# Optimization experiments

Measured on AMD Instinct MI355X. Metric: run time of the kernel, lower is better.

Reference implementation:

```python
import jax, jax.numpy as jnp
import numpy as np

B, S, D = 8, 4096, 512
EPS = 1e-6


def setup_inputs() -> dict:
    key = jax.random.key(0)
    ks = jax.random.split(key, 9)
    scale = 1.0 / np.sqrt(D)
    inp = {
        "x_seq": jax.random.normal(ks[0], (B, S, D), dtype=jnp.float32),
        "Wq": jax.random.uniform(ks[1], (D, D), jnp.float32, -scale, scale),
        "bq": jax.random.uniform(ks[2], (D,), jnp.float32, -scale, scale),
        "Wk": jax.random.uniform(ks[3], (D, D), jnp.float32, -scale, scale),
        "bk": jax.random.uniform(ks[4], (D,), jnp.float32, -scale, scale),
        "Wv": jax.random.uniform(ks[5], (D, D), jnp.float32, -scale, scale),
        "bv": jax.random.uniform(ks[6], (D,), jnp.float32, -scale, scale),
        "Wa": jax.random.uniform(ks[7], (D, D), jnp.float32, -scale, scale),
        "ba": jax.random.uniform(ks[8], (D,), jnp.float32, -scale, scale),
    }
    return inp


def _forward(x_seq, Wq, bq, Wk, bk, Wv, bv, Wa, ba):
    # Precompute all projections for the whole sequence (big GEMMs).
    q = jax.nn.relu(jnp.einsum('bsd,ed->bse', x_seq, Wq) + bq)  # phi = relu
    k = jax.nn.relu(jnp.einsum('bsd,ed->bse', x_seq, Wk) + bk)
    v = jnp.einsum('bsd,ed->bse', x_seq, Wv) + bv
    a = jax.nn.sigmoid(jnp.einsum('bsd,ed->bse', x_seq, Wa) + ba)

    # time-major for scan: (S, B, D)
    qs, ks_, vs, as_ = (jnp.swapaxes(t, 0, 1) for t in (q, k, v, a))

    def step(carry, inp):
        s, z = carry                      # s: (B,D,D), z: (B,D)
        q_t, k_t, v_t, a_t = inp
        s = a_t[:, :, None] * s + k_t[:, :, None] * v_t[:, None, :]
        z = a_t * z + k_t
        num = jnp.einsum('bi,bij->bj', q_t, s)
        den = jnp.sum(q_t * z, axis=-1, keepdims=True) + EPS
        return (s, z), num / den

    s0 = jnp.zeros((x_seq.shape[0], x_seq.shape[2], x_seq.shape[2]), x_seq.dtype)
    z0 = jnp.zeros((x_seq.shape[0], x_seq.shape[2]), x_seq.dtype)
    _, ys = jax.lax.scan(step, (s0, z0), (qs, ks_, vs, as_))
    return jnp.swapaxes(ys, 0, 1)  # (B, S, D)


def reference(x_seq, Wq, bq, Wk, bk, Wv, bv, Wa, ba):
    return _forward(x_seq, Wq, bq, Wk, bk, Wv, bv, Wa, ba)
```

## Files before the change

### kernel.cpp

```cpp
#include <hip/hip_runtime.h>
#include <hip/hip_bf16.h>
#include <cstdint>
#include <cstddef>

#define D_DIM 512
#define B_DIM 8
#define S_DIM 4096
#define M_DIM (B_DIM * S_DIM)
#define CHUNK 64
#define NCHUNK (S_DIM / CHUNK)
#define NSEG 8
#define CSEG (NCHUNK / NSEG)
#define EPS_C 1e-6f

typedef __attribute__((ext_vector_type(8))) short bf16x8;
typedef __attribute__((ext_vector_type(4))) float f32x4;

#define GLOAD_LDS16(src, dst)                                              \
  __builtin_amdgcn_global_load_lds(                                        \
      (const __attribute__((address_space(1))) void*)(src),                \
      (__attribute__((address_space(3))) void*)(dst), 16, 0, 0)

__device__ __forceinline__ unsigned short f2bf(float f) {
  uint32_t u = __float_as_uint(f);
  u = (u + 0x7fffu + ((u >> 16) & 1u)) >> 16;
  return (unsigned short)u;
}
__device__ __forceinline__ float bf2f(unsigned short s) { return __uint_as_float(((uint32_t)s) << 16); }

__global__ void cvt_f32_bf16(const float* __restrict__ in, unsigned short* __restrict__ out, int n4) {
  int i = blockIdx.x * blockDim.x + threadIdx.x;
  int stride = gridDim.x * blockDim.x;
  for (; i < n4; i += stride) {
    float4 f = ((const float4*)in)[i];
    ushort4 o;
    o.x = f2bf(f.x); o.y = f2bf(f.y); o.z = f2bf(f.z); o.w = f2bf(f.w);
    ((ushort4*)out)[i] = o;
  }
}

#define PTM 256
#define PTN 256
#define PBK 64

__global__ __launch_bounds__(512, 2) void proj_gemm(
    const unsigned short* __restrict__ Xb,
    const unsigned short* __restrict__ Wb,
    const float* __restrict__ bq, const float* __restrict__ bk,
    const float* __restrict__ bv, const float* __restrict__ ba,
    unsigned short* __restrict__ q_ws, unsigned short* __restrict__ k_ws,
    unsigned short* __restrict__ v_ws, unsigned short* __restrict__ g_ws) {
  __shared__ unsigned short SB[2 * (PTM + PTN) * PBK];

  const int proj = blockIdx.z;
  const unsigned short* W = Wb + (size_t)proj * D_DIM * D_DIM;
  const int m0 = blockIdx.x * PTM;
  const int n0 = blockIdx.y * PTN;
  const int lane = threadIdx.x & 63;
  const int w = threadIdx.x >> 6;
  const int l16 = lane & 15, q4 = lane >> 4;
  const int wm = (w >> 2) * 128;
  const int wn = (w & 3) * 64;

  f32x4 acc[8][4];
#pragma unroll
  for (int m = 0; m < 8; ++m)
#pragma unroll
    for (int n = 0; n < 4; ++n) acc[m][n] = (f32x4){0.f, 0.f, 0.f, 0.f};

  const int srow = lane >> 3;
  const int sg = lane & 7;

  auto STAGE = [&](int buf, int kc) {
    unsigned short* A = SB + buf * ((PTM + PTN) * PBK);
    unsigned short* Bs = A + PTM * PBK;
#pragma unroll
    for (int q = 0; q < 4; ++q) {
      const int row = w * 32 + q * 8 + srow;
      const int g = sg ^ (row & 7);
      GLOAD_LDS16(&Xb[(size_t)(m0 + row) * D_DIM + kc + g * 8], &A[(w * 32 + q * 8) * PBK]);
      GLOAD_LDS16(&W[(size_t)(n0 + row) * D_DIM + kc + g * 8], &Bs[(w * 32 + q * 8) * PBK]);
    }
  };

  STAGE(0, 0);
  __syncthreads();

  for (int t = 0; t < D_DIM / PBK; ++t) {
    const int cur = t & 1;
    if (t + 1 < D_DIM / PBK) STAGE(cur ^ 1, (t + 1) * PBK);

    const unsigned short* A = SB + cur * ((PTM + PTN) * PBK);
    const unsigned short* Bs = A + PTM * PBK;
    const int rsw = l16 & 7;
#pragma unroll
    for (int ks = 0; ks < 2; ++ks) {
      const int gphys = ((ks * 4 + q4) ^ rsw) * 8;
      bf16x8 afr[8], bfr[4];
#pragma unroll
      for (int m = 0; m < 8; ++m)
        afr[m] = *(const bf16x8*)&A[(wm + m * 16 + l16) * PBK + gphys];
#pragma unroll
      for (int n = 0; n < 4; ++n)
        bfr[n] = *(const bf16x8*)&Bs[(wn + n * 16 + l16) * PBK + gphys];
#pragma unroll
      for (int m = 0; m < 8; ++m)
#pragma unroll
        for (int n = 0; n < 4; ++n)
          acc[m][n] = __builtin_amdgcn_mfma_f32_16x16x32_bf16(afr[m], bfr[n], acc[m][n], 0, 0, 0);
    }
    __syncthreads();
  }

  const float* bias = (proj == 0) ? bq : (proj == 1) ? bk : (proj == 2) ? bv : ba;
  unsigned short* outp = (proj == 0) ? q_ws : (proj == 1) ? k_ws : (proj == 2) ? v_ws : g_ws;
  const bool do_relu = (proj <= 1);
  unsigned short* EP = &SB[w * 128 * 32];

#pragma unroll
  for (int p = 0; p < 2; ++p) {
#pragma unroll
    for (int half = 0; half < 2; ++half) {
      const int in_idx = p * 2 + half;
      const int nn = n0 + wn + in_idx * 16 + l16;
      const float bn = bias[nn];
#pragma unroll
      for (int m = 0; m < 8; ++m) {
#pragma unroll
        for (int vv = 0; vv < 4; ++vv) {
          float val = acc[m][in_idx][vv] + bn;
          if (do_relu) val = fmaxf(val, 0.f);
          EP[(m * 16 + q4 * 4 + vv) * 32 + half * 16 + l16] = f2bf(val);
        }
      }
    }
#pragma unroll
    for (int it = 0; it < 8; ++it) {
      const int row = it * 16 + (lane >> 2);
      const int ccol = (lane & 3) * 8;
      bf16x8 vdat = *(const bf16x8*)&EP[row * 32 + ccol];
      size_t gidx = (size_t)(m0 + wm + row) * D_DIM + (size_t)(n0 + wn + p * 32 + ccol);
      *(bf16x8*)&outp[gidx] = vdat;
    }
  }
}

__global__ __launch_bounds__(512) void prep(
    const unsigned short* __restrict__ q, const unsigned short* __restrict__ k,
    const unsigned short* __restrict__ g,
    unsigned short* __restrict__ qt, unsigned short* __restrict__ kt,
    unsigned short* __restrict__ kh,
    float* __restrict__ Af, float* __restrict__ khs) {
  __shared__ float segp[8][512];
  const int c = blockIdx.x, b = blockIdx.y;
  const int seg = threadIdx.x >> 6;
  const int t = threadIdx.x & 63;
  const int i0 = t * 8;
  const int r0 = seg * 8;
  const size_t t0 = (size_t)b * S_DIM + (size_t)c * CHUNK;
  const size_t cb = ((size_t)b * NCHUNK + c) * D_DIM;

  float sp[8];
#pragma unroll
  for (int j = 0; j < 8; ++j) sp[j] = 1.f;
  for (int r = 0; r < 8; ++r) {
    bf16x8 gv = *(const bf16x8*)&g[(t0 + r0 + r) * D_DIM + i0];
#pragma unroll
    for (int j = 0; j < 8; ++j)
      sp[j] *= 1.f / (1.f + __expf(-bf2f((unsigned short)gv[j])));
  }
  *(float4*)&segp[seg][i0] = *(float4*)&sp[0];
  *(float4*)&segp[seg][i0 + 4] = *(float4*)&sp[4];
  __syncthreads();

  float pre[8], tot[8];
#pragma unroll
  for (int j = 0; j < 8; ++j) { pre[j] = 1.f; tot[j] = 1.f; }
  for (int s2 = 0; s2 < 8; ++s2) {
    float4 v0 = *(const float4*)&segp[s2][i0];
    float4 v1 = *(const float4*)&segp[s2][i0 + 4];
    float v[8] = {v0.x, v0.y, v0.z, v0.w, v1.x, v1.y, v1.z, v1.w};
#pragma unroll
    for (int j = 0; j < 8; ++j) {
      tot[j] *= v[j];
      if (s2 < seg) pre[j] *= v[j];
    }
  }
  if (seg == 0) {
    float4 a0 = {tot[0], tot[1], tot[2], tot[3]};
    float4 a1 = {tot[4], tot[5], tot[6], tot[7]};
    *(float4*)&Af[cb + i0] = a0;
    *(float4*)&Af[cb + i0 + 4] = a1;
  }

  float cum[8], ssum[8];
#pragma unroll
  for (int j = 0; j < 8; ++j) { cum[j] = pre[j]; ssum[j] = 0.f; }
  for (int r = 0; r < 8; ++r) {
    size_t idx = (t0 + r0 + r) * D_DIM + i0;
    bf16x8 gv = *(const bf16x8*)&g[idx];
    bf16x8 qv8 = *(const bf16x8*)&q[idx];
    bf16x8 kv8 = *(const bf16x8*)&k[idx];
    bf16x8 oq, ok, okh;
#pragma unroll
    for (int j = 0; j < 8; ++j) {
      cum[j] *= 1.f / (1.f + __expf(-bf2f((unsigned short)gv[j])));
      float qv = bf2f((unsigned short)qv8[j]);
      float kv = bf2f((unsigned short)kv8[j]);
      oq[j] = (short)f2bf(qv * cum[j]);
      float inv = 1.f / cum[j];
      ok[j] = (short)f2bf(kv * inv);
      float khf = kv * (tot[j] * inv);
      okh[j] = (short)f2bf(khf);
      ssum[j] += khf;
    }
    *(bf16x8*)&qt[idx] = oq;
    *(bf16x8*)&kt[idx] = ok;
    *(bf16x8*)&kh[idx] = okh;
  }

  __syncthreads();
  *(float4*)&segp[seg][i0] = *(float4*)&ssum[0];
  *(float4*)&segp[seg][i0 + 4] = *(float4*)&ssum[4];
  __syncthreads();
  if (seg == 0) {
    float s[8];
#pragma unroll
    for (int j = 0; j < 8; ++j) s[j] = 0.f;
    for (int s2 = 0; s2 < 8; ++s2) {
      float4 v0 = *(const float4*)&segp[s2][i0];
      float4 v1 = *(const float4*)&segp[s2][i0 + 4];
      s[0] += v0.x; s[1] += v0.y; s[2] += v0.z; s[3] += v0.w;
      s[4] += v1.x; s[5] += v1.y; s[6] += v1.z; s[7] += v1.w;
    }
    float4 a0 = {s[0], s[1], s[2], s[3]};
    float4 a1 = {s[4], s[5], s[6], s[7]};
    *(float4*)&khs[cb + i0] = a0;
    *(float4*)&khs[cb + i0 + 4] = a1;
  }
}

__global__ __launch_bounds__(256) void transpose_cd(
    const unsigned short* __restrict__ in, unsigned short* __restrict__ outT) {
  __shared__ unsigned short tile[CHUNK][264];
  const int c = blockIdx.x, b = blockIdx.y;
  const size_t base_in = ((size_t)b * S_DIM + (size_t)c * CHUNK) * D_DIM;
  const size_t base_out = ((size_t)b * NCHUNK + c) * (size_t)D_DIM * CHUNK;
  const int tid = threadIdx.x;
#pragma unroll
  for (int h = 0; h < 2; ++h) {
    if (h) __syncthreads();
#pragma unroll
    for (int it = 0; it < 8; ++it) {
      int flat = (it * 256 + tid) * 8;
      int row = flat >> 8;
      int col = flat & 255;
      *(uint4*)&tile[row][col] = *(const uint4*)&in[base_in + (size_t)row * D_DIM + h * 256 + col];
    }
    __syncthreads();
#pragma unroll
    for (int it = 0; it < 8; ++it) {
      int wq = it * 256 + tid;
      int i_loc = wq >> 3;
      int r0 = (wq & 7) * 8;
      ushort4 v0, v1;
      v0.x = tile[r0 + 0][i_loc]; v0.y = tile[r0 + 1][i_loc];
      v0.z = tile[r0 + 2][i_loc]; v0.w = tile[r0 + 3][i_loc];
      v1.x = tile[r0 + 4][i_loc]; v1.y = tile[r0 + 5][i_loc];
      v1.z = tile[r0 + 6][i_loc]; v1.w = tile[r0 + 7][i_loc];
      size_t o = base_out + (size_t)(h * 256 + i_loc) * CHUNK + r0;
      *(ushort4*)&outT[o] = v0;
      *(ushort4*)&outT[o + 4] = v1;
    }
  }
}

__global__ __launch_bounds__(256) void intra(
    const unsigned short* __restrict__ qt, const unsigned short* kt,
    const unsigned short* __restrict__ VT,
    unsigned short* numI, float* __restrict__ rs) {
  __shared__ unsigned short P_lds[CHUNK][CHUNK + 8];
  const int c = blockIdx.x, b = blockIdx.y;
  const size_t t0 = (size_t)b * S_DIM + (size_t)c * CHUNK;
  const int lane = threadIdx.x & 63, w = threadIdx.x >> 6;
  const int l16 = lane & 15, q4 = lane >> 4;

  f32x4 accP[4];
#pragma unroll
  for (int n = 0; n < 4; ++n) accP[n] = (f32x4){0.f, 0.f, 0.f, 0.f};
#pragma unroll
  for (int ks = 0; ks < 16; ++ks) {
    bf16x8 afr = *(const bf16x8*)&qt[(t0 + 16 * w + l16) * D_DIM + 32 * ks + 8 * q4];
#pragma unroll
    for (int n = 0; n < 4; ++n) {
      bf16x8 bfr = *(const bf16x8*)&kt[(t0 + 16 * n + l16) * D_DIM + 32 * ks + 8 * q4];
      accP[n] = __builtin_amdgcn_mfma_f32_16x16x32_bf16(afr, bfr, accP[n], 0, 0, 0);
    }
  }
  float rsum[4] = {0.f, 0.f, 0.f, 0.f};
#pragma unroll
  for (int n = 0; n < 4; ++n) {
    int m = 16 * n + l16;
#pragma unroll
    for (int vv = 0; vv < 4; ++vv) {
      int r = 16 * w + 4 * q4 + vv;
      float pv = (m <= r) ? accP[n][vv] : 0.f;
      rsum[vv] += pv;
      P_lds[r][m] = f2bf(pv);
    }
  }
#pragma unroll
  for (int msk = 1; msk < 16; msk <<= 1) {
#pragma unroll
    for (int vv = 0; vv < 4; ++vv) rsum[vv] += __shfl_xor(rsum[vv], msk, 64);
  }
  if (l16 == 0) {
#pragma unroll
    for (int vv = 0; vv < 4; ++vv) rs[t0 + 16 * w + 4 * q4 + vv] = rsum[vv];
  }
  __syncthreads();
  bf16x8 pa0 = *(const bf16x8*)&P_lds[16 * w + l16][8 * q4];
  bf16x8 pa1 = *(const bf16x8*)&P_lds[16 * w + l16][32 + 8 * q4];
  const size_t vtb = ((size_t)b * NCHUNK + c) * (size_t)D_DIM * CHUNK;
#pragma unroll 4
  for (int nt = 0; nt < 32; ++nt) {
    bf16x8 b0 = *(const bf16x8*)&VT[vtb + (size_t)(nt * 16 + l16) * CHUNK + 8 * q4];
    bf16x8 b1 = *(const bf16x8*)&VT[vtb + (size_t)(nt * 16 + l16) * CHUNK + 32 + 8 * q4];
    f32x4 acc = (f32x4){0.f, 0.f, 0.f, 0.f};
    acc = __builtin_amdgcn_mfma_f32_16x16x32_bf16(pa0, b0, acc, 0, 0, 0);
    acc = __builtin_amdgcn_mfma_f32_16x16x32_bf16(pa1, b1, acc, 0, 0, 0);
#pragma unroll
    for (int vv = 0; vv < 4; ++vv)
      numI[(t0 + 16 * w + 4 * q4 + vv) * D_DIM + nt * 16 + l16] = f2bf(acc[vv]);
  }
}

__global__ __launch_bounds__(512) void zscan(
    const float* __restrict__ Af, const float* __restrict__ khs,
    float* __restrict__ zall, float* __restrict__ Pseg) {
  const int b = blockIdx.x;
  const int i = threadIdx.x;
  float z = 0.f, rp = 1.f;
  for (int c = 0; c < NCHUNK; ++c) {
    const size_t cb = ((size_t)b * NCHUNK + c) * D_DIM;
    zall[cb + i] = z;
    float af = Af[cb + i];
    z = fmaf(af, z, khs[cb + i]);
    rp *= af;
    if ((c & (CSEG - 1)) == CSEG - 1) {
      Pseg[((size_t)b * NSEG + (c / CSEG)) * D_DIM + i] = rp;
      rp = 1.f;
    }
  }
}

__global__ __launch_bounds__(512) void denk(
    const unsigned short* __restrict__ qt, const float* __restrict__ zall,
    float* rs_invden) {
  const int c = blockIdx.x, b = blockIdx.y;
  const int lane = threadIdx.x & 63, w = threadIdx.x >> 6;
  const size_t t0 = (size_t)b * S_DIM + (size_t)c * CHUNK;
  const size_t zb = ((size_t)b * NCHUNK + c) * D_DIM;
  float4 z0 = *(const float4*)&zall[zb + lane * 8];
  float4 z1 = *(const float4*)&zall[zb + lane * 8 + 4];
#pragma unroll
  for (int rr = 0; rr < 8; ++rr) {
    int r = 8 * w + rr;
    bf16x8 qv = *(const bf16x8*)&qt[(t0 + r) * D_DIM + lane * 8];
    float p = 0.f;
    p = fmaf(bf2f((unsigned short)qv[0]), z0.x, p);
    p = fmaf(bf2f((unsigned short)qv[1]), z0.y, p);
    p = fmaf(bf2f((unsigned short)qv[2]), z0.z, p);
    p = fmaf(bf2f((unsigned short)qv[3]), z0.w, p);
    p = fmaf(bf2f((unsigned short)qv[4]), z1.x, p);
    p = fmaf(bf2f((unsigned short)qv[5]), z1.y, p);
    p = fmaf(bf2f((unsigned short)qv[6]), z1.z, p);
    p = fmaf(bf2f((unsigned short)qv[7]), z1.w, p);
#pragma unroll
    for (int msk = 1; msk < 64; msk <<= 1) p += __shfl_xor(p, msk, 64);
    if (lane == 0) {
      float* iv = &rs_invden[t0 + r];
      *iv = 1.f / (p + *iv + EPS_C);
    }
  }
}

__global__ __launch_bounds__(512, 2) void useg_k(
    const unsigned short* __restrict__ khT, const unsigned short* __restrict__ VT,
    const float* __restrict__ Af, unsigned short* __restrict__ U) {
  __shared__ unsigned short VTl[2][128 * 64];
  const int s = blockIdx.x, jt = blockIdx.y, b = blockIdx.z;
  const int lane = threadIdx.x & 63, w = threadIdx.x >> 6;
  const int l16 = lane & 15, q4 = lane >> 4;
  const int j0 = jt * 128;
  const int iw = 64 * w;
  const int vrow = lane >> 3;
  const int vswz = (lane & 7) ^ (vrow & 7);

  f32x4 acc[4][8];
#pragma unroll
  for (int T = 0; T < 4; ++T)
#pragma unroll
    for (int h = 0; h < 8; ++h) acc[T][h] = (f32x4){0.f, 0.f, 0.f, 0.f};

  const size_t cb0 = ((size_t)b * NCHUNK + s * CSEG) * D_DIM;
  {
    const size_t ob0 = cb0 * CHUNK;
#pragma unroll
    for (int kk = 0; kk < 2; ++kk) {
      const int k = 2 * w + kk;
      GLOAD_LDS16(&VT[ob0 + (size_t)(j0 + 8 * k + vrow) * CHUNK + vswz * 8],
                  &VTl[0][k * 512]);
    }
  }
  bf16x8 a0[4], a1[4];
  {
    const size_t ob0 = cb0 * CHUNK;
#pragma unroll
    for (int T = 0; T < 4; ++T) {
      a0[T] = *(const bf16x8*)&khT[ob0 + (size_t)(iw + 16 * T + l16) * CHUNK + 8 * q4];
      a1[T] = *(const bf16x8*)&khT[ob0 + (size_t)(iw + 16 * T + l16) * CHUNK + 32 + 8 * q4];
    }
  }

  for (int cc = 0; cc < CSEG; ++cc) {
    const size_t cb = cb0 + (size_t)cc * D_DIM;
    __syncthreads();
    if (cc + 1 < CSEG) {
      const size_t obn = (cb + D_DIM) * CHUNK;
#pragma unroll
      for (int kk = 0; kk < 2; ++kk) {
        const int k = 2 * w + kk;
        GLOAD_LDS16(&VT[obn + (size_t)(j0 + 8 * k + vrow) * CHUNK + vswz * 8],
                    &VTl[(cc + 1) & 1][k * 512]);
      }
    }
#pragma unroll
    for (int T = 0; T < 4; ++T) {
      float4 af = *(const float4*)&Af[cb + iw + 16 * T + 4 * q4];
#pragma unroll
      for (int h = 0; h < 8; ++h) {
        acc[T][h][0] *= af.x; acc[T][h][1] *= af.y; acc[T][h][2] *= af.z; acc[T][h][3] *= af.w;
      }
    }
    const unsigned short* Vb = VTl[cc & 1];
#pragma unroll
    for (int h = 0; h < 8; ++h) {
      const int jpos = 16 * h + l16;
      const int swz = jpos & 7;
      bf16x8 bv0 = *(const bf16x8*)&Vb[jpos * 64 + ((q4 ^ swz) * 8)];
      bf16x8 bv1 = *(const bf16x8*)&Vb[jpos * 64 + (((4 + q4) ^ swz) * 8)];
#pragma unroll
      for (int T = 0; T < 4; ++T) {
        acc[T][h] = __builtin_amdgcn_mfma_f32_16x16x32_bf16(a0[T], bv0, acc[T][h], 0, 0, 0);
        acc[T][h] = __builtin_amdgcn_mfma_f32_16x16x32_bf16(a1[T], bv1, acc[T][h], 0, 0, 0);
      }
    }
    if (cc + 1 < CSEG) {
      const size_t obn = (cb + D_DIM) * CHUNK;
#pragma unroll
      for (int T = 0; T < 4; ++T) {
        a0[T] = *(const bf16x8*)&khT[obn + (size_t)(iw + 16 * T + l16) * CHUNK + 8 * q4];
        a1[T] = *(const bf16x8*)&khT[obn + (size_t)(iw + 16 * T + l16) * CHUNK + 32 + 8 * q4];
      }
    }
  }
  const size_t ub = ((size_t)b * NSEG + s) * D_DIM;
#pragma unroll
  for (int T = 0; T < 4; ++T)
#pragma unroll
    for (int h = 0; h < 8; ++h) {
      uint2 pk;
      pk.x = (uint32_t)f2bf(acc[T][h][0]) | ((uint32_t)f2bf(acc[T][h][1]) << 16);
      pk.y = (uint32_t)f2bf(acc[T][h][2]) | ((uint32_t)f2bf(acc[T][h][3]) << 16);
      *(uint2*)&U[(ub + j0 + 16 * h + l16) * (size_t)D_DIM + iw + 16 * T + 4 * q4] = pk;
    }
}

__global__ __launch_bounds__(256) void sscan(
    const float* __restrict__ Pseg, unsigned short* __restrict__ U) {
  const int b = blockIdx.y;
  const int flat = blockIdx.x * 256 + threadIdx.x;
  const int j = flat >> 6;
  const int i0 = (flat & 63) * 8;
  float acc[8];
#pragma unroll
  for (int t = 0; t < 8; ++t) acc[t] = 0.f;
  for (int s = 0; s < NSEG; ++s) {
    const size_t pb = ((size_t)b * NSEG + s) * D_DIM;
    unsigned short* up = &U[(pb + j) * (size_t)D_DIM + i0];
    uint4 u = *(const uint4*)up;
    float4 p0 = *(const float4*)&Pseg[pb + i0];
    float4 p1 = *(const float4*)&Pseg[pb + i0 + 4];
    float uv[8];
    uv[0] = bf2f((unsigned short)(u.x & 0xffff)); uv[1] = bf2f((unsigned short)(u.x >> 16));
    uv[2] = bf2f((unsigned short)(u.y & 0xffff)); uv[3] = bf2f((unsigned short)(u.y >> 16));
    uv[4] = bf2f((unsigned short)(u.z & 0xffff)); uv[5] = bf2f((unsigned short)(u.z >> 16));
    uv[6] = bf2f((unsigned short)(u.w & 0xffff)); uv[7] = bf2f((unsigned short)(u.w >> 16));
    uint4 o;
    o.x = (uint32_t)f2bf(acc[0]) | ((uint32_t)f2bf(acc[1]) << 16);
    o.y = (uint32_t)f2bf(acc[2]) | ((uint32_t)f2bf(acc[3]) << 16);
    o.z = (uint32_t)f2bf(acc[4]) | ((uint32_t)f2bf(acc[5]) << 16);
    o.w = (uint32_t)f2bf(acc[6]) | ((uint32_t)f2bf(acc[7]) << 16);
    *(uint4*)up = o;
    acc[0] = fmaf(p0.x, acc[0], uv[0]);
    acc[1] = fmaf(p0.y, acc[1], uv[1]);
    acc[2] = fmaf(p0.z, acc[2], uv[2]);
    acc[3] = fmaf(p0.w, acc[3], uv[3]);
    acc[4] = fmaf(p1.x, acc[4], uv[4]);
    acc[5] = fmaf(p1.y, acc[5], uv[5]);
    acc[6] = fmaf(p1.z, acc[6], uv[6]);
    acc[7] = fmaf(p1.w, acc[7], uv[7]);
  }
}

__global__ __launch_bounds__(512, 2) void scan2(
    const unsigned short* __restrict__ qt, const unsigned short* __restrict__ khT,
    const unsigned short* __restrict__ VT, const float* __restrict__ Af,
    const unsigned short* __restrict__ Sin,
    const unsigned short* __restrict__ numI, const float* __restrict__ invden,
    float* __restrict__ out) {
  __shared__ unsigned short STj[128][520];
  __shared__ unsigned short VTl[128 * 64];
  const int s = blockIdx.x, jt = blockIdx.y, b = blockIdx.z;
  const int lane = threadIdx.x & 63, w = threadIdx.x >> 6;
  const int l16 = lane & 15, q4 = lane >> 4;
  const int j0 = jt * 128;
  const int iw = 64 * w;
  const int rw = 16 * (w & 3);
  const int jo = 64 * (w >> 2);
  const int vrow = lane >> 3;
  const int vswz = (lane & 7) ^ (vrow & 7);

  f32x4 acc[4][8];

  {
    const size_t pb = ((size_t)b * NSEG + s) * D_DIM;
#pragma unroll
    for (int T = 0; T < 4; ++T)
#pragma unroll
      for (int h = 0; h < 8; ++h) {
        uint2 uu = *(const uint2*)&Sin[(pb + j0 + 16 * h + l16) * (size_t)D_DIM + iw + 16 * T + 4 * q4];
        acc[T][h][0] = bf2f((unsigned short)(uu.x & 0xffff));
        acc[T][h][1] = bf2f((unsigned short)(uu.x >> 16));
        acc[T][h][2] = bf2f((unsigned short)(uu.y & 0xffff));
        acc[T][h][3] = bf2f((unsigned short)(uu.y >> 16));
      }
  }

  for (int cc = 0; cc < CSEG; ++cc) {
    const int c = s * CSEG + cc;
    const size_t cb = ((size_t)b * NCHUNK + c) * D_DIM;
    const size_t t0 = (size_t)b * S_DIM + (size_t)c * CHUNK;
    const size_t ob = cb * CHUNK;
    const bool upd = (cc != CSEG - 1);

    bf16x8 a0[4], a1[4];
    if (upd) {
#pragma unroll
      for (int kk = 0; kk < 2; ++kk) {
        const int k = 2 * w + kk;
        GLOAD_LDS16(&VT[ob + (size_t)(j0 + 8 * k + vrow) * CHUNK + vswz * 8],
                    &VTl[k * 512]);
      }
#pragma unroll
      for (int T = 0; T < 4; ++T) {
        a0[T] = *(const bf16x8*)&khT[ob + (size_t)(iw + 16 * T + l16) * CHUNK + 8 * q4];
        a1[T] = *(const bf16x8*)&khT[ob + (size_t)(iw + 16 * T + l16) * CHUNK + 32 + 8 * q4];
      }
    }

#pragma unroll
    for (int T = 0; T < 4; ++T)
#pragma unroll
      for (int h = 0; h < 8; ++h) {
        uint2 pk;
        pk.x = (uint32_t)f2bf(acc[T][h][0]) | ((uint32_t)f2bf(acc[T][h][1]) << 16);
        pk.y = (uint32_t)f2bf(acc[T][h][2]) | ((uint32_t)f2bf(acc[T][h][3]) << 16);
        *(uint2*)&STj[16 * h + l16][iw + 16 * T + 4 * q4] = pk;
      }
    __syncthreads();

    {
      f32x4 accO[4];
#pragma unroll
      for (int h = 0; h < 4; ++h) accO[h] = (f32x4){0.f, 0.f, 0.f, 0.f};
#pragma unroll
      for (int ks = 0; ks < 16; ++ks) {
        bf16x8 afr = *(const bf16x8*)&qt[(t0 + rw + l16) * D_DIM + 32 * ks + 8 * q4];
#pragma unroll
        for (int h = 0; h < 4; ++h) {
          bf16x8 bfr = *(const bf16x8*)&STj[jo + 16 * h + l16][32 * ks + 8 * q4];
          accO[h] = __builtin_amdgcn_mfma_f32_16x16x32_bf16(afr, bfr, accO[h], 0, 0, 0);
        }
      }
#pragma unroll
      for (int h = 0; h < 4; ++h)
#pragma unroll
        for (int vv = 0; vv < 4; ++vv) {
          size_t t = t0 + rw + 4 * q4 + vv;
          int j = j0 + jo + 16 * h + l16;
          float idv = invden[t];
          float nI = bf2f(numI[t * D_DIM + j]);
          out[t * D_DIM + j] = (accO[h][vv] + nI) * idv;
        }
    }

    if (upd) {
#pragma unroll
      for (int T = 0; T < 4; ++T) {
        float4 af = *(const float4*)&Af[cb + iw + 16 * T + 4 * q4];
#pragma unroll
        for (int h = 0; h < 8; ++h) {
          acc[T][h][0] *= af.x; acc[T][h][1] *= af.y; acc[T][h][2] *= af.z; acc[T][h][3] *= af.w;
        }
      }
#pragma unroll
      for (int h = 0; h < 8; ++h) {
        const int jpos = 16 * h + l16;
        const int swz = jpos & 7;
        bf16x8 bv0 = *(const bf16x8*)&VTl[jpos * 64 + ((q4 ^ swz) * 8)];
        bf16x8 bv1 = *(const bf16x8*)&VTl[jpos * 64 + (((4 + q4) ^ swz) * 8)];
#pragma unroll
        for (int T = 0; T < 4; ++T) {
          acc[T][h] = __builtin_amdgcn_mfma_f32_16x16x32_bf16(a0[T], bv0, acc[T][h], 0, 0, 0);
          acc[T][h] = __builtin_amdgcn_mfma_f32_16x16x32_bf16(a1[T], bv1, acc[T][h], 0, 0, 0);
        }
      }
    }
    __syncthreads();
  }
}

extern "C" void kernel_launch(void* const* d_in, const int* in_sizes, int n_in,
                              void* d_out, int out_size, void* d_ws, size_t ws_size,
                              hipStream_t stream) {
  const float* x  = (const float*)d_in[0];
  const float* Wq = (const float*)d_in[1];
  const float* bq = (const float*)d_in[2];
  const float* Wk = (const float*)d_in[3];
  const float* bk = (const float*)d_in[4];
  const float* Wv = (const float*)d_in[5];
  const float* bv = (const float*)d_in[6];
  const float* Wa = (const float*)d_in[7];
  const float* ba = (const float*)d_in[8];
  float* out = (float*)d_out;

  const size_t MD2 = (size_t)M_DIM * D_DIM * 2;
  uint8_t* w = (uint8_t*)d_ws;
  unsigned short* xb   = (unsigned short*)w; w += MD2;
  unsigned short* wb   = (unsigned short*)w; w += (size_t)4 * D_DIM * D_DIM * 2;
  unsigned short* q_ws = (unsigned short*)w; w += MD2;
  unsigned short* k_ws = (unsigned short*)w; w += MD2;
  unsigned short* v_ws = (unsigned short*)w; w += MD2;
  unsigned short* g_ws = (unsigned short*)w; w += MD2;
  float* Af     = (float*)w; w += (size_t)B_DIM * NCHUNK * D_DIM * 4;
  float* khs    = (float*)w; w += (size_t)B_DIM * NCHUNK * D_DIM * 4;
  float* invden = (float*)w; w += (size_t)M_DIM * 4;

  unsigned short* qt   = xb;
  unsigned short* kt   = q_ws;
  unsigned short* kh   = k_ws;
  unsigned short* VT   = g_ws;
  unsigned short* khT  = v_ws;
  unsigned short* numI = q_ws;
  unsigned short* U    = k_ws;
  float* zall = (float*)wb;
  float* Pseg = (float*)((uint8_t*)wb + (1 << 20));

  cvt_f32_bf16<<<1024, 256, 0, stream>>>(x, xb, M_DIM * D_DIM / 4);
  cvt_f32_bf16<<<128, 256, 0, stream>>>(Wq, wb + 0 * D_DIM * D_DIM, D_DIM * D_DIM / 4);
  cvt_f32_bf16<<<128, 256, 0, stream>>>(Wk, wb + 1 * D_DIM * D_DIM, D_DIM * D_DIM / 4);
  cvt_f32_bf16<<<128, 256, 0, stream>>>(Wv, wb + 2 * D_DIM * D_DIM, D_DIM * D_DIM / 4);
  cvt_f32_bf16<<<128, 256, 0, stream>>>(Wa, wb + 3 * D_DIM * D_DIM, D_DIM * D_DIM / 4);

  proj_gemm<<<dim3(M_DIM / PTM, D_DIM / PTN, 4), 512, 0, stream>>>(
      xb, wb, bq, bk, bv, ba, q_ws, k_ws, v_ws, g_ws);

  prep<<<dim3(NCHUNK, B_DIM), 512, 0, stream>>>(q_ws, k_ws, g_ws, qt, kt, kh, Af, khs);
  transpose_cd<<<dim3(NCHUNK, B_DIM), 256, 0, stream>>>(v_ws, VT);
  transpose_cd<<<dim3(NCHUNK, B_DIM), 256, 0, stream>>>(kh, khT);
  zscan<<<B_DIM, 512, 0, stream>>>(Af, khs, zall, Pseg);
  intra<<<dim3(NCHUNK, B_DIM), 256, 0, stream>>>(qt, kt, VT, numI, invden);
  denk<<<dim3(NCHUNK, B_DIM), 512, 0, stream>>>(qt, zall, invden);
  useg_k<<<dim3(NSEG, 4, B_DIM), 512, 0, stream>>>(khT, VT, Af, U);
  sscan<<<dim3(128, B_DIM), 256, 0, stream>>>(Pseg, U);
  scan2<<<dim3(NSEG, 4, B_DIM), 512, 0, stream>>>(qt, khT, VT, Af, U, numI, invden, out);
}
```

Measured before the change: 508.3 us.

## Fuse denominator into intra kernel, widen zscan grid, register-prefetch V tiles

Removes the separate denk kernel by computing the q·z dot product inside the intra kernel from an LDS copy of z, so the row sums never round-trip through global memory. zscan is split across 4 blocks per batch instead of one, which spreads the serial chunk scan over more CUs. In useg_k and scan2, the async global-to-LDS V loads are replaced by register prefetch plus ds_write, behind explicit lgkmcnt waits and barriers. scan2 also prefetches the next chunk's khT and V operands across the loop. These changes save a kernel launch and aim to overlap global loads with MFMA work, at the cost of extra register pressure.

After: 496.5 us. -2.3%, faster.

```diff
diff --git a/kernel.cpp b/kernel.cpp
--- a/kernel.cpp
+++ b/kernel.cpp
@@ -20,6 +20,13 @@
   __builtin_amdgcn_global_load_lds(                                        \
       (const __attribute__((address_space(1))) void*)(src),                \
       (__attribute__((address_space(3))) void*)(dst), 16, 0, 0)
+
+#define LGKM_BARRIER()                                                     \
+  do {                                                                     \
+    asm volatile("s_waitcnt lgkmcnt(0)" ::: "memory");                     \
+    __builtin_amdgcn_s_barrier();                                          \
+    __builtin_amdgcn_sched_barrier(0);                                     \
+  } while (0)
 
 __device__ __forceinline__ unsigned short f2bf(float f) {
   uint32_t u = __float_as_uint(f);
@@ -277,20 +284,31 @@
 
 __global__ __launch_bounds__(256) void intra(
     const unsigned short* __restrict__ qt, const unsigned short* kt,
-    const unsigned short* __restrict__ VT,
-    unsigned short* numI, float* __restrict__ rs) {
+    const unsigned short* __restrict__ VT, const float* __restrict__ zall,
+    unsigned short* numI, float* __restrict__ invden) {
   __shared__ unsigned short P_lds[CHUNK][CHUNK + 8];
+  __shared__ float zl[512];
+  __shared__ float rsl[64];
   const int c = blockIdx.x, b = blockIdx.y;
   const size_t t0 = (size_t)b * S_DIM + (size_t)c * CHUNK;
+  const size_t zb = ((size_t)b * NCHUNK + c) * D_DIM;
   const int lane = threadIdx.x & 63, w = threadIdx.x >> 6;
   const int l16 = lane & 15, q4 = lane >> 4;
 
+  zl[threadIdx.x] = zall[zb + threadIdx.x];
+  zl[threadIdx.x + 256] = zall[zb + threadIdx.x + 256];
+  __syncthreads();
+
   f32x4 accP[4];
 #pragma unroll
   for (int n = 0; n < 4; ++n) accP[n] = (f32x4){0.f, 0.f, 0.f, 0.f};
+  float qdotz = 0.f;
 #pragma unroll
   for (int ks = 0; ks < 16; ++ks) {
     bf16x8 afr = *(const bf16x8*)&qt[(t0 + 16 * w + l16) * D_DIM + 32 * ks + 8 * q4];
+    const float* zp = &zl[32 * ks + 8 * q4];
+#pragma unroll
+    for (int j = 0; j < 8; ++j) qdotz = fmaf(bf2f((unsigned short)afr[j]), zp[j], qdotz);
 #pragma unroll
     for (int n = 0; n < 4; ++n) {
       bf16x8 bfr = *(const bf16x8*)&kt[(t0 + 16 * n + l16) * D_DIM + 32 * ks + 8 * q4];
@@ -316,9 +334,15 @@
   }
   if (l16 == 0) {
 #pragma unroll
-    for (int vv = 0; vv < 4; ++vv) rs[t0 + 16 * w + 4 * q4 + vv] = rsum[vv];
+    for (int vv = 0; vv < 4; ++vv) rsl[16 * w + 4 * q4 + vv] = rsum[vv];
   }
   __syncthreads();
+
+  qdotz += __shfl_xor(qdotz, 16, 64);
+  qdotz += __shfl_xor(qdotz, 32, 64);
+  if (q4 == 0)
+    invden[t0 + 16 * w + l16] = 1.f / (qdotz + rsl[16 * w + l16] + EPS_C);
+
   bf16x8 pa0 = *(const bf16x8*)&P_lds[16 * w + l16][8 * q4];
   bf16x8 pa1 = *(const bf16x8*)&P_lds[16 * w + l16][32 + 8 * q4];
   const size_t vtb = ((size_t)b * NCHUNK + c) * (size_t)D_DIM * CHUNK;
@@ -335,11 +359,11 @@
   }
 }
 
-__global__ __launch_bounds__(512) void zscan(
+__global__ __launch_bounds__(128) void zscan(
     const float* __restrict__ Af, const float* __restrict__ khs,
     float* __restrict__ zall, float* __restrict__ Pseg) {
-  const int b = blockIdx.x;
-  const int i = threadIdx.x;
+  const int b = blockIdx.y;
+  const int i = blockIdx.x * 128 + threadIdx.x;
   float z = 0.f, rp = 1.f;
   for (int c = 0; c < NCHUNK; ++c) {
     const size_t cb = ((size_t)b * NCHUNK + c) * D_DIM;
@@ -354,37 +378,6 @@
   }
 }
 
-__global__ __launch_bounds__(512) void denk(
-    const unsigned short* __restrict__ qt, const float* __restrict__ zall,
-    float* rs_invden) {
-  const int c = blockIdx.x, b = blockIdx.y;
-  const int lane = threadIdx.x & 63, w = threadIdx.x >> 6;
-  const size_t t0 = (size_t)b * S_DIM + (size_t)c * CHUNK;
-  const size_t zb = ((size_t)b * NCHUNK + c) * D_DIM;
-  float4 z0 = *(const float4*)&zall[zb + lane * 8];
-  float4 z1 = *(const float4*)&zall[zb + lane * 8 + 4];
-#pragma unroll
-  for (int rr = 0; rr < 8; ++rr) {
-    int r = 8 * w + rr;
-    bf16x8 qv = *(const bf16x8*)&qt[(t0 + r) * D_DIM + lane * 8];
-    float p = 0.f;
-    p = fmaf(bf2f((unsigned short)qv[0]), z0.x, p);
-    p = fmaf(bf2f((unsigned short)qv[1]), z0.y, p);
-    p = fmaf(bf2f((unsigned short)qv[2]), z0.z, p);
-    p = fmaf(bf2f((unsigned short)qv[3]), z0.w, p);
-    p = fmaf(bf2f((unsigned short)qv[4]), z1.x, p);
-    p = fmaf(bf2f((unsigned short)qv[5]), z1.y, p);
-    p = fmaf(bf2f((unsigned short)qv[6]), z1.z, p);
-    p = fmaf(bf2f((unsigned short)qv[7]), z1.w, p);
-#pragma unroll
-    for (int msk = 1; msk < 64; msk <<= 1) p += __shfl_xor(p, msk, 64);
-    if (lane == 0) {
-      float* iv = &rs_invden[t0 + r];
-      *iv = 1.f / (p + *iv + EPS_C);
-    }
-  }
-}
-
 __global__ __launch_bounds__(512, 2) void useg_k(
     const unsigned short* __restrict__ khT, const unsigned short* __restrict__ VT,
     const float* __restrict__ Af, unsigned short* __restrict__ U) {
@@ -395,7 +388,8 @@
   const int j0 = jt * 128;
   const int iw = 64 * w;
   const int vrow = lane >> 3;
-  const int vswz = (lane & 7) ^ (vrow & 7);
+  const int vg = lane & 7;
+  const int vgl = vg ^ vrow;
 
   f32x4 acc[4][8];
 #pragma unroll
@@ -404,36 +398,27 @@
     for (int h = 0; h < 8; ++h) acc[T][h] = (f32x4){0.f, 0.f, 0.f, 0.f};
 
   const size_t cb0 = ((size_t)b * NCHUNK + s * CSEG) * D_DIM;
+  bf16x8 vb0, vb1, a0[4], a1[4];
   {
     const size_t ob0 = cb0 * CHUNK;
-#pragma unroll
-    for (int kk = 0; kk < 2; ++kk) {
-      const int k = 2 * w + kk;
-      GLOAD_LDS16(&VT[ob0 + (size_t)(j0 + 8 * k + vrow) * CHUNK + vswz * 8],
-                  &VTl[0][k * 512]);
-    }
-  }
-  bf16x8 a0[4], a1[4];
-  {
-    const size_t ob0 = cb0 * CHUNK;
+    vb0 = *(const bf16x8*)&VT[ob0 + (size_t)(j0 + 16 * w + vrow) * CHUNK + vgl * 8];
+    vb1 = *(const bf16x8*)&VT[ob0 + (size_t)(j0 + 16 * w + 8 + vrow) * CHUNK + vgl * 8];
 #pragma unroll
     for (int T = 0; T < 4; ++T) {
       a0[T] = *(const bf16x8*)&khT[ob0 + (size_t)(iw + 16 * T + l16) * CHUNK + 8 * q4];
       a1[T] = *(const bf16x8*)&khT[ob0 + (size_t)(iw + 16 * T + l16) * CHUNK + 32 + 8 * q4];
     }
-  }
+    *(bf16x8*)&VTl[0][(16 * w + vrow) * 64 + vg * 8] = vb0;
+    *(bf16x8*)&VTl[0][(16 * w + 8 + vrow) * 64 + vg * 8] = vb1;
+  }
+  LGKM_BARRIER();
 
   for (int cc = 0; cc < CSEG; ++cc) {
     const size_t cb = cb0 + (size_t)cc * D_DIM;
-    __syncthreads();
+    const size_t obn = (cb + D_DIM) * CHUNK;
     if (cc + 1 < CSEG) {
-      const size_t obn = (cb + D_DIM) * CHUNK;
-#pragma unroll
-      for (int kk = 0; kk < 2; ++kk) {
-        const int k = 2 * w + kk;
-        GLOAD_LDS16(&VT[obn + (size_t)(j0 + 8 * k + vrow) * CHUNK + vswz * 8],
-                    &VTl[(cc + 1) & 1][k * 512]);
-      }
+      vb0 = *(const bf16x8*)&VT[obn + (size_t)(j0 + 16 * w + vrow) * CHUNK + vgl * 8];
+      vb1 = *(const bf16x8*)&VT[obn + (size_t)(j0 + 16 * w + 8 + vrow) * CHUNK + vgl * 8];
     }
 #pragma unroll
     for (int T = 0; T < 4; ++T) {
@@ -457,13 +442,16 @@
       }
     }
     if (cc + 1 < CSEG) {
-      const size_t obn = (cb + D_DIM) * CHUNK;
+      unsigned short* Vn = VTl[(cc + 1) & 1];
+      *(bf16x8*)&Vn[(16 * w + vrow) * 64 + vg * 8] = vb0;
+      *(bf16x8*)&Vn[(16 * w + 8 + vrow) * 64 + vg * 8] = vb1;
 #pragma unroll
       for (int T = 0; T < 4; ++T) {
         a0[T] = *(const bf16x8*)&khT[obn + (size_t)(iw + 16 * T + l16) * CHUNK + 8 * q4];
         a1[T] = *(const bf16x8*)&khT[obn + (size_t)(iw + 16 * T + l16) * CHUNK + 32 + 8 * q4];
       }
     }
+    LGKM_BARRIER();
   }
   const size_t ub = ((size_t)b * NSEG + s) * D_DIM;
 #pragma unroll
@@ -530,7 +518,8 @@
   const int rw = 16 * (w & 3);
   const int jo = 64 * (w >> 2);
   const int vrow = lane >> 3;
-  const int vswz = (lane & 7) ^ (vrow & 7);
+  const int vg = lane & 7;
+  const int vgl = vg ^ vrow;
 
   f32x4 acc[4][8];
 
@@ -548,6 +537,18 @@
       }
   }
 
+  bf16x8 vb0, vb1, a0[4], a1[4];
+  {
+    const size_t ob0 = ((size_t)b * NCHUNK + s * CSEG) * D_DIM * CHUNK;
+    vb0 = *(const bf16x8*)&VT[ob0 + (size_t)(j0 + 16 * w + vrow) * CHUNK + vgl * 8];
+    vb1 = *(const bf16x8*)&VT[ob0 + (size_t)(j0 + 16 * w + 8 + vrow) * CHUNK + vgl * 8];
+#pragma unroll
+    for (int T = 0; T < 4; ++T) {
+      a0[T] = *(const bf16x8*)&khT[ob0 + (size_t)(iw + 16 * T + l16) * CHUNK + 8 * q4];
+      a1[T] = *(const bf16x8*)&khT[ob0 + (size_t)(iw + 16 * T + l16) * CHUNK + 32 + 8 * q4];
+    }
+  }
+
   for (int cc = 0; cc < CSEG; ++cc) {
     const int c = s * CSEG + cc;
     const size_t cb = ((size_t)b * NCHUNK + c) * D_DIM;
@@ -555,21 +556,6 @@
     const size_t ob = cb * CHUNK;
     const bool upd = (cc != CSEG - 1);
 
-    bf16x8 a0[4], a1[4];
-    if (upd) {
-#pragma unroll
-      for (int kk = 0; kk < 2; ++kk) {
-        const int k = 2 * w + kk;
-        GLOAD_LDS16(&VT[ob + (size_t)(j0 + 8 * k + vrow) * CHUNK + vswz * 8],
-                    &VTl[k * 512]);
-      }
-#pragma unroll
-      for (int T = 0; T < 4; ++T) {
-        a0[T] = *(const bf16x8*)&khT[ob + (size_t)(iw + 16 * T + l16) * CHUNK + 8 * q4];
-        a1[T] = *(const bf16x8*)&khT[ob + (size_t)(iw + 16 * T + l16) * CHUNK + 32 + 8 * q4];
-      }
-    }
-
 #pragma unroll
     for (int T = 0; T < 4; ++T)
 #pragma unroll
@@ -579,7 +565,17 @@
         pk.y = (uint32_t)f2bf(acc[T][h][2]) | ((uint32_t)f2bf(acc[T][h][3]) << 16);
         *(uint2*)&STj[16 * h + l16][iw + 16 * T + 4 * q4] = pk;
       }
-    __syncthreads();
+    if (upd) {
+      *(bf16x8*)&VTl[(16 * w + vrow) * 64 + vg * 8] = vb0;
+      *(bf16x8*)&VTl[(16 * w + 8 + vrow) * 64 + vg * 8] = vb1;
+    }
+    LGKM_BARRIER();
+
+    if (cc < CSEG - 2) {
+      const size_t obn = ob + (size_t)D_DIM * CHUNK;
+      vb0 = *(const bf16x8*)&VT[obn + (size_t)(j0 + 16 * w + vrow) * CHUNK + vgl * 8];
+      vb1 = *(const bf16x8*)&VT[obn + (size_t)(j0 + 16 * w + 8 + vrow) * CHUNK + vgl * 8];
+    }
 
     {
       f32x4 accO[4];
@@ -628,7 +624,15 @@
         }
       }
     }
-    __syncthreads();
+    if (cc < CSEG - 2) {
+      const size_t obn = ob + (size_t)D_DIM * CHUNK;
+#pragma unroll
+      for (int T = 0; T < 4; ++T) {
+        a0[T] = *(const bf16x8*)&khT[obn + (size_t)(iw + 16 * T + l16) * CHUNK + 8 * q4];
+        a1[T] = *(const bf16x8*)&khT[obn + (size_t)(iw + 16 * T + l16) * CHUNK + 32 + 8 * q4];
+      }
+    }
+    LGKM_BARRIER();
   }
 }
 
@@ -680,9 +684,8 @@
   prep<<<dim3(NCHUNK, B_DIM), 512, 0, stream>>>(q_ws, k_ws, g_ws, qt, kt, kh, Af, khs);
   transpose_cd<<<dim3(NCHUNK, B_DIM), 256, 0, stream>>>(v_ws, VT);
   transpose_cd<<<dim3(NCHUNK, B_DIM), 256, 0, stream>>>(kh, khT);
-  zscan<<<B_DIM, 512, 0, stream>>>(Af, khs, zall, Pseg);
-  intra<<<dim3(NCHUNK, B_DIM), 256, 0, stream>>>(qt, kt, VT, numI, invden);
-  denk<<<dim3(NCHUNK, B_DIM), 512, 0, stream>>>(qt, zall, invden);
+  zscan<<<dim3(4, B_DIM), 128, 0, stream>>>(Af, khs, zall, Pseg);
+  intra<<<dim3(NCHUNK, B_DIM), 256, 0, stream>>>(qt, kt, VT, zall, numI, invden);
   useg_k<<<dim3(NSEG, 4, B_DIM), 512, 0, stream>>>(khT, VT, Af, U);
   sscan<<<dim3(128, B_DIM), 256, 0, stream>>>(Pseg, U);
   scan2<<<dim3(NSEG, 4, B_DIM), 512, 0, stream>>>(qt, khT, VT, Af, U, numI, invden, out);
```
